# Optimization experiments

Measured on AMD Instinct MI355X. Metric: run time of the kernel, lower is better.

Reference implementation:

```python
import jax, jax.numpy as jnp
import numpy as np

B, NF, QUERY_DIM = 4, 300, 512
HIDDEN, NUM_HEADS = 512, 8
H, W = 80, 80
HEAD_DIM = HIDDEN // NUM_HEADS
NORM_FACT = float(HIDDEN / NUM_HEADS) ** (-0.5)


def setup_inputs() -> dict:
    key = jax.random.key(0)
    k1, k2, k3, k4, k5 = jax.random.split(key, 5)
    # xavier_uniform bound for [HIDDEN, QUERY_DIM] weight
    bound = float(np.sqrt(6.0 / (HIDDEN + QUERY_DIM)))
    return {
        "q": jax.random.normal(k1, (B, NF, QUERY_DIM), dtype=jnp.float32),
        "k": jax.random.normal(k2, (B, QUERY_DIM, H, W), dtype=jnp.float32),
        "mask": jax.random.bernoulli(k3, 0.25, (B, H, W)),  # True = masked out
        "q_w": jax.random.uniform(k4, (HIDDEN, QUERY_DIM), jnp.float32, -bound, bound),
        "q_b": jnp.zeros((HIDDEN,), jnp.float32),
        "k_w": jax.random.uniform(k5, (HIDDEN, QUERY_DIM), jnp.float32, -bound, bound),
        "k_b": jnp.zeros((HIDDEN,), jnp.float32),
    }


def reference(q, k, mask, q_w, q_b, k_w, k_b):
    b, nf, _ = q.shape
    h, w = k.shape[-2], k.shape[-1]
    # q projection: [b, nf, hidden]
    qp = jnp.einsum("bqd,ed->bqe", q, q_w) + q_b
    # k projection (1x1 conv == channel matmul): [b, hidden, h, w]
    kp = jnp.einsum("bdhw,ed->behw", k, k_w) + k_b[None, :, None, None]
    # split heads
    qh = qp.reshape(b, nf, NUM_HEADS, HEAD_DIM) * NORM_FACT   # [b,q,n,c]
    kh = kp.reshape(b, NUM_HEADS, HEAD_DIM, h, w)             # [b,n,c,h,w]
    # batched QK scores (replaces the per-query python loop + cat(dim=2))
    weights = jnp.einsum("bqnc,bnchw->bqnhw", qh, kh)
    weights = weights.reshape(b, 1, nf * NUM_HEADS, h, w)
    # masked_fill with -inf on padded spatial positions
    weights = jnp.where(mask[:, None, None, :, :], -jnp.inf, weights)
    # NOTE: softmax over flatten(2) = jointly over (queries*heads*h*w), as in source
    weights = jax.nn.softmax(weights.reshape(b, 1, -1), axis=-1)
    return weights.reshape(b, 1, nf * NUM_HEADS, h, w)
```

## Files before the change

kernel.cpp:

```cpp
#include <hip/hip_runtime.h>
#include <math.h>

#define B_    4
#define NF    300
#define QD    512
#define HID   512
#define NH    8
#define HD    64
#define HW    6400
#define ROWS  2400
#define PB    15360000
#define NORM_FACT 0.125f
#define NEG_INF (-INFINITY)
#define LDK   40

typedef __bf16 bf16_t;
typedef __bf16 bf16x4_t __attribute__((ext_vector_type(4)));
typedef __bf16 bf16x8_t __attribute__((ext_vector_type(8)));
typedef float  f32x4    __attribute__((ext_vector_type(4)));

__device__ __forceinline__ void splitf(float x, bf16_t& h, bf16_t& l) {
    h = (bf16_t)x;
    l = (bf16_t)(x - (float)h);
}

__global__ __launch_bounds__(256) void qproj_kernel(
    const float* __restrict__ q, const float* __restrict__ qw,
    const float* __restrict__ qb, float* __restrict__ qh)
{
    __shared__ float qs[4][QD];
    const int r0 = blockIdx.x * 4;
    const int t  = threadIdx.x;
    #pragma unroll
    for (int row = 0; row < 4; ++row) {
        qs[row][t]       = q[(size_t)(r0 + row) * QD + t];
        qs[row][t + 256] = q[(size_t)(r0 + row) * QD + t + 256];
    }
    __syncthreads();
    #pragma unroll
    for (int eo = 0; eo < 2; ++eo) {
        const int e = t + eo * 256;
        float a0 = 0.f, a1 = 0.f, a2 = 0.f, a3 = 0.f;
        for (int d = 0; d < QD; d += 4) {
            float4 w = *(const float4*)&qw[(size_t)e * QD + d];
            a0 += qs[0][d]*w.x + qs[0][d+1]*w.y + qs[0][d+2]*w.z + qs[0][d+3]*w.w;
            a1 += qs[1][d]*w.x + qs[1][d+1]*w.y + qs[1][d+2]*w.z + qs[1][d+3]*w.w;
            a2 += qs[2][d]*w.x + qs[2][d+1]*w.y + qs[2][d+2]*w.z + qs[2][d+3]*w.w;
            a3 += qs[3][d]*w.x + qs[3][d+1]*w.y + qs[3][d+2]*w.z + qs[3][d+3]*w.w;
        }
        const float bias = qb[e];
        qh[(size_t)(r0+0)*HID + e] = (a0 + bias) * NORM_FACT;
        qh[(size_t)(r0+1)*HID + e] = (a1 + bias) * NORM_FACT;
        qh[(size_t)(r0+2)*HID + e] = (a2 + bias) * NORM_FACT;
        qh[(size_t)(r0+3)*HID + e] = (a3 + bias) * NORM_FACT;
    }
}

__global__ __launch_bounds__(256) void kproj_mfma(
    const float* __restrict__ k, const float* __restrict__ kw,
    const float* __restrict__ kb, float* __restrict__ kp)
{
    __shared__ __align__(16) bf16_t Ah[128][LDK];
    __shared__ __align__(16) bf16_t Al[128][LDK];
    __shared__ __align__(16) bf16_t Bh[128][LDK];
    __shared__ __align__(16) bf16_t Bl[128][LDK];
    const int b  = blockIdx.z;
    const int e0 = blockIdx.y * 128;
    const int p0 = blockIdx.x * 128;
    const int t  = threadIdx.x;
    const int wave = t >> 6, lane = t & 63;
    const int wr = wave >> 1, wc = wave & 1;
    const int lm = lane & 15, lq = lane >> 4;
    const float* kB = k + (size_t)b * QD * HW;

    f32x4 acc[4][4];
    const f32x4 zero4 = {0.f, 0.f, 0.f, 0.f};
    #pragma unroll
    for (int i = 0; i < 4; ++i)
        #pragma unroll
        for (int j = 0; j < 4; ++j) acc[i][j] = zero4;

    for (int d0 = 0; d0 < QD; d0 += 32) {
        #pragma unroll
        for (int i = 0; i < 4; ++i) {
            int idx = t + i * 256;
            int e = idx >> 3, dp = (idx & 7) << 2;
            float4 v = *(const float4*)&kw[(size_t)(e0 + e) * QD + d0 + dp];
            bf16x4_t hv, lv; bf16_t hx, lx;
            splitf(v.x, hx, lx); hv[0] = hx; lv[0] = lx;
            splitf(v.y, hx, lx); hv[1] = hx; lv[1] = lx;
            splitf(v.z, hx, lx); hv[2] = hx; lv[2] = lx;
            splitf(v.w, hx, lx); hv[3] = hx; lv[3] = lx;
            *(bf16x4_t*)&Ah[e][dp] = hv;
            *(bf16x4_t*)&Al[e][dp] = lv;
        }
        #pragma unroll
        for (int i = 0; i < 4; ++i) {
            int idx = t + i * 256;
            int p = idx & 127, db = (idx >> 7) << 2;
            bf16x4_t hv, lv;
            #pragma unroll
            for (int j = 0; j < 4; ++j) {
                float x = kB[(size_t)(d0 + db + j) * HW + p0 + p];
                bf16_t hx, lx; splitf(x, hx, lx);
                hv[j] = hx; lv[j] = lx;
            }
            *(bf16x4_t*)&Bh[p][db] = hv;
            *(bf16x4_t*)&Bl[p][db] = lv;
        }
        __syncthreads();

        bf16x8_t ah[4], al[4], bh[4], bl[4];
        #pragma unroll
        for (int mt = 0; mt < 4; ++mt) {
            int r = wr * 64 + mt * 16 + lm;
            ah[mt] = *(const bf16x8_t*)&Ah[r][lq * 8];
            al[mt] = *(const bf16x8_t*)&Al[r][lq * 8];
        }
        #pragma unroll
        for (int nt = 0; nt < 4; ++nt) {
            int c = wc * 64 + nt * 16 + lm;
            bh[nt] = *(const bf16x8_t*)&Bh[c][lq * 8];
            bl[nt] = *(const bf16x8_t*)&Bl[c][lq * 8];
        }
        #pragma unroll
        for (int mt = 0; mt < 4; ++mt)
            #pragma unroll
            for (int nt = 0; nt < 4; ++nt) {
                f32x4 a = acc[mt][nt];
                a = __builtin_amdgcn_mfma_f32_16x16x32_bf16(al[mt], bh[nt], a, 0, 0, 0);
                a = __builtin_amdgcn_mfma_f32_16x16x32_bf16(ah[mt], bl[nt], a, 0, 0, 0);
                a = __builtin_amdgcn_mfma_f32_16x16x32_bf16(ah[mt], bh[nt], a, 0, 0, 0);
                acc[mt][nt] = a;
            }
        __syncthreads();
    }

    #pragma unroll
    for (int mt = 0; mt < 4; ++mt) {
        #pragma unroll
        for (int reg = 0; reg < 4; ++reg) {
            int e = e0 + wr * 64 + mt * 16 + lq * 4 + reg;
            float bias = kb[e];
            float* dst = kp + (size_t)b * HID * HW + (size_t)e * HW + p0 + wc * 64 + lm;
            #pragma unroll
            for (int nt = 0; nt < 4; ++nt)
                dst[nt * 16] = acc[mt][nt][reg] + bias;
        }
    }
}

__global__ __launch_bounds__(256) void scores_pass_a(
    const float* __restrict__ qh, const float* __restrict__ kp,
    const int* __restrict__ mask, float* __restrict__ partials)
{
    __shared__ __align__(16) bf16_t Ah[128][LDK];
    __shared__ __align__(16) bf16_t Bh[128][LDK];
    __shared__ float redM[256];
    __shared__ float redS[256];
    const int z  = blockIdx.z;
    const int b  = z >> 3, n = z & 7;
    const int q0 = blockIdx.y * 128;
    const int p0 = blockIdx.x * 128;
    const int t  = threadIdx.x;
    const int wave = t >> 6, lane = t & 63;
    const int wr = wave >> 1, wc = wave & 1;
    const int lm = lane & 15, lq = lane >> 4;

    f32x4 acc[4][4];
    const f32x4 zero4 = {0.f, 0.f, 0.f, 0.f};
    #pragma unroll
    for (int i = 0; i < 4; ++i)
        #pragma unroll
        for (int j = 0; j < 4; ++j) acc[i][j] = zero4;

    for (int d0 = 0; d0 < HD; d0 += 32) {
        #pragma unroll
        for (int i = 0; i < 4; ++i) {
            int idx = t + i * 256;
            int qq = idx >> 3, dp = (idx & 7) << 2;
            int qg = q0 + qq;
            float4 v = make_float4(0.f, 0.f, 0.f, 0.f);
            if (qg < NF)
                v = *(const float4*)&qh[(size_t)(b * NF + qg) * HID + n * HD + d0 + dp];
            bf16x4_t hv;
            hv[0] = (bf16_t)v.x; hv[1] = (bf16_t)v.y;
            hv[2] = (bf16_t)v.z; hv[3] = (bf16_t)v.w;
            *(bf16x4_t*)&Ah[qq][dp] = hv;
        }
        const float* kpB = kp + (size_t)b * HID * HW + (size_t)(n * HD + d0) * HW;
        #pragma unroll
        for (int i = 0; i < 4; ++i) {
            int idx = t + i * 256;
            int p = idx & 127, db = (idx >> 7) << 2;
            bf16x4_t hv;
            #pragma unroll
            for (int j = 0; j < 4; ++j)
                hv[j] = (bf16_t)kpB[(size_t)(db + j) * HW + p0 + p];
            *(bf16x4_t*)&Bh[p][db] = hv;
        }
        __syncthreads();

        bf16x8_t ah[4], bh[4];
        #pragma unroll
        for (int mt = 0; mt < 4; ++mt)
            ah[mt] = *(const bf16x8_t*)&Ah[wr * 64 + mt * 16 + lm][lq * 8];
        #pragma unroll
        for (int nt = 0; nt < 4; ++nt)
            bh[nt] = *(const bf16x8_t*)&Bh[wc * 64 + nt * 16 + lm][lq * 8];
        #pragma unroll
        for (int mt = 0; mt < 4; ++mt)
            #pragma unroll
            for (int nt = 0; nt < 4; ++nt)
                acc[mt][nt] = __builtin_amdgcn_mfma_f32_16x16x32_bf16(
                    ah[mt], bh[nt], acc[mt][nt], 0, 0, 0);
        __syncthreads();
    }

    int mm[4];
    #pragma unroll
    for (int nt = 0; nt < 4; ++nt)
        mm[nt] = mask[b * HW + p0 + wc * 64 + nt * 16 + lm];

    float tm = NEG_INF;
    #pragma unroll
    for (int mt = 0; mt < 4; ++mt) {
        int qbase = q0 + wr * 64 + mt * 16 + lq * 4;
        #pragma unroll
        for (int reg = 0; reg < 4; ++reg) {
            if (qbase + reg < NF) {
                #pragma unroll
                for (int nt = 0; nt < 4; ++nt)
                    if (!mm[nt]) tm = fmaxf(tm, acc[mt][nt][reg]);
            }
        }
    }
    float ts = 0.f;
    if (tm != NEG_INF) {
        #pragma unroll
        for (int mt = 0; mt < 4; ++mt) {
            int qbase = q0 + wr * 64 + mt * 16 + lq * 4;
            #pragma unroll
            for (int reg = 0; reg < 4; ++reg) {
                if (qbase + reg < NF) {
                    #pragma unroll
                    for (int nt = 0; nt < 4; ++nt)
                        if (!mm[nt]) ts += __expf(acc[mt][nt][reg] - tm);
                }
            }
        }
    }

    redM[t] = tm; redS[t] = ts;
    __syncthreads();
    for (int off = 128; off > 0; off >>= 1) {
        if (t < off) {
            float m1 = redM[t],       s1 = redS[t];
            float m2 = redM[t + off], s2 = redS[t + off];
            float M = fmaxf(m1, m2);
            float s = (M == NEG_INF) ? 0.f
                      : (s1 * __expf(m1 - M) + s2 * __expf(m2 - M));
            redM[t] = M; redS[t] = s;
        }
        __syncthreads();
    }
    if (t == 0) {
        int lin = (z * gridDim.y + blockIdx.y) * gridDim.x + blockIdx.x;
        partials[2 * lin]     = redM[0];
        partials[2 * lin + 1] = redS[0];
    }
}

__global__ __launch_bounds__(256) void stats_kernel(
    const float* __restrict__ partials, float* __restrict__ stats, int nper)
{
    __shared__ float redM[256];
    __shared__ float redS[256];
    const int b = blockIdx.x, t = threadIdx.x;
    const float* p = partials + (size_t)b * nper * 2;
    float m = NEG_INF, s = 0.f;
    for (int i = t; i < nper; i += 256) {
        float m2 = p[2 * i], s2 = p[2 * i + 1];
        float M = fmaxf(m, m2);
        float ns = (M == NEG_INF) ? 0.f
                   : (s * __expf(m - M) + s2 * __expf(m2 - M));
        m = M; s = ns;
    }
    redM[t] = m; redS[t] = s;
    __syncthreads();
    for (int off = 128; off > 0; off >>= 1) {
        if (t < off) {
            float m1 = redM[t],       s1 = redS[t];
            float m2 = redM[t + off], s2 = redS[t + off];
            float M = fmaxf(m1, m2);
            float ns = (M == NEG_INF) ? 0.f
                       : (s1 * __expf(m1 - M) + s2 * __expf(m2 - M));
            redM[t] = M; redS[t] = ns;
        }
        __syncthreads();
    }
    if (t == 0) {
        stats[2 * b]     = redM[0];
        stats[2 * b + 1] = 1.0f / redS[0];
    }
}

__global__ __launch_bounds__(256) void scores_pass_b(
    const float* __restrict__ qh, const float* __restrict__ kp,
    const int* __restrict__ mask, const float* __restrict__ stats,
    float* __restrict__ out)
{
    __shared__ __align__(16) bf16_t Ah[128][LDK];
    __shared__ __align__(16) bf16_t Al[128][LDK];
    __shared__ __align__(16) bf16_t Bh[128][LDK];
    __shared__ __align__(16) bf16_t Bl[128][LDK];
    const int z  = blockIdx.z;
    const int b  = z >> 3, n = z & 7;
    const int q0 = blockIdx.y * 128;
    const int p0 = blockIdx.x * 128;
    const int t  = threadIdx.x;
    const int wave = t >> 6, lane = t & 63;
    const int wr = wave >> 1, wc = wave & 1;
    const int lm = lane & 15, lq = lane >> 4;

    const float M    = stats[2 * b];
    const float invS = stats[2 * b + 1];

    f32x4 acc[4][4];
    const f32x4 zero4 = {0.f, 0.f, 0.f, 0.f};
    #pragma unroll
    for (int i = 0; i < 4; ++i)
        #pragma unroll
        for (int j = 0; j < 4; ++j) acc[i][j] = zero4;

    for (int d0 = 0; d0 < HD; d0 += 32) {
        #pragma unroll
        for (int i = 0; i < 4; ++i) {
            int idx = t + i * 256;
            int qq = idx >> 3, dp = (idx & 7) << 2;
            int qg = q0 + qq;
            float4 v = make_float4(0.f, 0.f, 0.f, 0.f);
            if (qg < NF)
                v = *(const float4*)&qh[(size_t)(b * NF + qg) * HID + n * HD + d0 + dp];
            bf16x4_t hv, lv; bf16_t hx, lx;
            splitf(v.x, hx, lx); hv[0] = hx; lv[0] = lx;
            splitf(v.y, hx, lx); hv[1] = hx; lv[1] = lx;
            splitf(v.z, hx, lx); hv[2] = hx; lv[2] = lx;
            splitf(v.w, hx, lx); hv[3] = hx; lv[3] = lx;
            *(bf16x4_t*)&Ah[qq][dp] = hv;
            *(bf16x4_t*)&Al[qq][dp] = lv;
        }
        const float* kpB = kp + (size_t)b * HID * HW + (size_t)(n * HD + d0) * HW;
        #pragma unroll
        for (int i = 0; i < 4; ++i) {
            int idx = t + i * 256;
            int p = idx & 127, db = (idx >> 7) << 2;
            bf16x4_t hv, lv;
            #pragma unroll
            for (int j = 0; j < 4; ++j) {
                float x = kpB[(size_t)(db + j) * HW + p0 + p];
                bf16_t hx, lx; splitf(x, hx, lx);
                hv[j] = hx; lv[j] = lx;
            }
            *(bf16x4_t*)&Bh[p][db] = hv;
            *(bf16x4_t*)&Bl[p][db] = lv;
        }
        __syncthreads();

        bf16x8_t ah[4], al[4], bh[4], bl[4];
        #pragma unroll
        for (int mt = 0; mt < 4; ++mt) {
            int r = wr * 64 + mt * 16 + lm;
            ah[mt] = *(const bf16x8_t*)&Ah[r][lq * 8];
            al[mt] = *(const bf16x8_t*)&Al[r][lq * 8];
        }
        #pragma unroll
        for (int nt = 0; nt < 4; ++nt) {
            int c = wc * 64 + nt * 16 + lm;
            bh[nt] = *(const bf16x8_t*)&Bh[c][lq * 8];
            bl[nt] = *(const bf16x8_t*)&Bl[c][lq * 8];
        }
        #pragma unroll
        for (int mt = 0; mt < 4; ++mt)
            #pragma unroll
            for (int nt = 0; nt < 4; ++nt) {
                f32x4 a = acc[mt][nt];
                a = __builtin_amdgcn_mfma_f32_16x16x32_bf16(al[mt], bh[nt], a, 0, 0, 0);
                a = __builtin_amdgcn_mfma_f32_16x16x32_bf16(ah[mt], bl[nt], a, 0, 0, 0);
                a = __builtin_amdgcn_mfma_f32_16x16x32_bf16(ah[mt], bh[nt], a, 0, 0, 0);
                acc[mt][nt] = a;
            }
        __syncthreads();
    }

    int mm[4];
    #pragma unroll
    for (int nt = 0; nt < 4; ++nt)
        mm[nt] = mask[b * HW + p0 + wc * 64 + nt * 16 + lm];

    #pragma unroll
    for (int mt = 0; mt < 4; ++mt) {
        #pragma unroll
        for (int reg = 0; reg < 4; ++reg) {
            int qg = q0 + wr * 64 + mt * 16 + lq * 4 + reg;
            if (qg < NF) {
                float* dst = out + (size_t)(b * ROWS + qg * NH + n) * HW + p0 + wc * 64 + lm;
                #pragma unroll
                for (int nt = 0; nt < 4; ++nt)
                    dst[nt * 16] = mm[nt] ? 0.f : __expf(acc[mt][nt][reg] - M) * invS;
            }
        }
    }
}

extern "C" void kernel_launch(void* const* d_in, const int* in_sizes, int n_in,
                              void* d_out, int out_size, void* d_ws, size_t ws_size,
                              hipStream_t stream) {
    const float* q    = (const float*)d_in[0];
    const float* k    = (const float*)d_in[1];
    const int*   mask = (const int*)  d_in[2];
    const float* qw   = (const float*)d_in[3];
    const float* qb   = (const float*)d_in[4];
    const float* kw   = (const float*)d_in[5];
    const float* kb   = (const float*)d_in[6];
    float* out = (float*)d_out;
    float* ws  = (float*)d_ws;

    float* qh       = ws;
    float* kp       = ws + 614400;
    float* partials = ws + 13721600;
    float* stats    = ws + 13731200;

    qproj_kernel<<<300, 256, 0, stream>>>(q, qw, qb, qh);
    kproj_mfma<<<dim3(50, 4, 4), 256, 0, stream>>>(k, kw, kb, kp);
    scores_pass_a<<<dim3(50, 3, 32), 256, 0, stream>>>(qh, kp, mask, partials);
    stats_kernel<<<4, 256, 0, stream>>>(partials, stats, 1200);
    scores_pass_b<<<dim3(50, 3, 32), 256, 0, stream>>>(qh, kp, mask, stats, out);
}
```

Baseline: 505.9 us.

## Emit pre-split bf16 head-major swizzled Q/K projections for direct tile loads

The q and k projection kernels now write their outputs as pre-split bf16 hi/lo arrays in a head-major, row-contiguous layout padded to 384 queries, with an XOR swizzle on the 64-wide channel dimension. The two score kernels then copy whole 128x64 tiles into LDS with 16-byte loads and read MFMA fragments through the matching swizzle. This removes the fp32-to-bf16 splitting and the column-strided global gathers that were repeated for every query block, and drops the per-K-step barriers. Pass A now reads only the hi half of the data. In exchange, the projection epilogues do scattered 2-byte stores, and the padded query rows are never written, so they stay uninitialised.

```diff
diff --git a/kernel.cpp b/kernel.cpp
--- a/kernel.cpp
+++ b/kernel.cpp
@@ -9,7 +9,7 @@
 #define HD    64
 #define HW    6400
 #define ROWS  2400
-#define PB    15360000
+#define NQP   384
 #define NORM_FACT 0.125f
 #define NEG_INF (-INFINITY)
 #define LDK   40
@@ -23,14 +23,20 @@
     h = (bf16_t)x;
     l = (bf16_t)(x - (float)h);
 }
+__device__ __forceinline__ int swz(int c, int row) {
+    return (((c >> 3) ^ (row & 7)) << 3) | (c & 7);
+}
 
 __global__ __launch_bounds__(256) void qproj_kernel(
     const float* __restrict__ q, const float* __restrict__ qw,
-    const float* __restrict__ qb, float* __restrict__ qh)
+    const float* __restrict__ qb, bf16_t* __restrict__ qh_hi,
+    bf16_t* __restrict__ qh_lo)
 {
     __shared__ float qs[4][QD];
-    const int r0 = blockIdx.x * 4;
-    const int t  = threadIdx.x;
+    const int r0    = blockIdx.x * 4;
+    const int b     = r0 / NF;
+    const int qbase = r0 % NF;
+    const int t     = threadIdx.x;
     #pragma unroll
     for (int row = 0; row < 4; ++row) {
         qs[row][t]       = q[(size_t)(r0 + row) * QD + t];
@@ -40,25 +46,31 @@
     #pragma unroll
     for (int eo = 0; eo < 2; ++eo) {
         const int e = t + eo * 256;
-        float a0 = 0.f, a1 = 0.f, a2 = 0.f, a3 = 0.f;
+        const int n = e >> 6, c = e & 63;
+        float a[4] = {0.f, 0.f, 0.f, 0.f};
         for (int d = 0; d < QD; d += 4) {
             float4 w = *(const float4*)&qw[(size_t)e * QD + d];
-            a0 += qs[0][d]*w.x + qs[0][d+1]*w.y + qs[0][d+2]*w.z + qs[0][d+3]*w.w;
-            a1 += qs[1][d]*w.x + qs[1][d+1]*w.y + qs[1][d+2]*w.z + qs[1][d+3]*w.w;
-            a2 += qs[2][d]*w.x + qs[2][d+1]*w.y + qs[2][d+2]*w.z + qs[2][d+3]*w.w;
-            a3 += qs[3][d]*w.x + qs[3][d+1]*w.y + qs[3][d+2]*w.z + qs[3][d+3]*w.w;
+            #pragma unroll
+            for (int row = 0; row < 4; ++row)
+                a[row] += qs[row][d]*w.x + qs[row][d+1]*w.y
+                        + qs[row][d+2]*w.z + qs[row][d+3]*w.w;
         }
         const float bias = qb[e];
-        qh[(size_t)(r0+0)*HID + e] = (a0 + bias) * NORM_FACT;
-        qh[(size_t)(r0+1)*HID + e] = (a1 + bias) * NORM_FACT;
-        qh[(size_t)(r0+2)*HID + e] = (a2 + bias) * NORM_FACT;
-        qh[(size_t)(r0+3)*HID + e] = (a3 + bias) * NORM_FACT;
+        #pragma unroll
+        for (int row = 0; row < 4; ++row) {
+            const int qq = qbase + row;
+            const float val = (a[row] + bias) * NORM_FACT;
+            bf16_t h, l; splitf(val, h, l);
+            size_t off = ((size_t)(b * NH + n) * NQP + qq) * 64 + swz(c, qq);
+            qh_hi[off] = h; qh_lo[off] = l;
+        }
     }
 }
 
 __global__ __launch_bounds__(256) void kproj_mfma(
     const float* __restrict__ k, const float* __restrict__ kw,
-    const float* __restrict__ kb, float* __restrict__ kp)
+    const float* __restrict__ kb, bf16_t* __restrict__ kp_hi,
+    bf16_t* __restrict__ kp_lo)
 {
     __shared__ __align__(16) bf16_t Ah[128][LDK];
     __shared__ __align__(16) bf16_t Al[128][LDK];
@@ -84,6 +96,20 @@
         #pragma unroll
         for (int i = 0; i < 4; ++i) {
             int idx = t + i * 256;
+            int p = idx & 127, db = (idx >> 7) << 2;
+            bf16x4_t hv, lv;
+            #pragma unroll
+            for (int j = 0; j < 4; ++j) {
+                float x = kB[(size_t)(d0 + db + j) * HW + p0 + p];
+                bf16_t hx, lx; splitf(x, hx, lx);
+                hv[j] = hx; lv[j] = lx;
+            }
+            *(bf16x4_t*)&Ah[p][db] = hv;
+            *(bf16x4_t*)&Al[p][db] = lv;
+        }
+        #pragma unroll
+        for (int i = 0; i < 4; ++i) {
+            int idx = t + i * 256;
             int e = idx >> 3, dp = (idx & 7) << 2;
             float4 v = *(const float4*)&kw[(size_t)(e0 + e) * QD + d0 + dp];
             bf16x4_t hv, lv; bf16_t hx, lx;
@@ -91,22 +117,8 @@
             splitf(v.y, hx, lx); hv[1] = hx; lv[1] = lx;
             splitf(v.z, hx, lx); hv[2] = hx; lv[2] = lx;
             splitf(v.w, hx, lx); hv[3] = hx; lv[3] = lx;
-            *(bf16x4_t*)&Ah[e][dp] = hv;
-            *(bf16x4_t*)&Al[e][dp] = lv;
-        }
-        #pragma unroll
-        for (int i = 0; i < 4; ++i) {
-            int idx = t + i * 256;
-            int p = idx & 127, db = (idx >> 7) << 2;
-            bf16x4_t hv, lv;
-            #pragma unroll
-            for (int j = 0; j < 4; ++j) {
-                float x = kB[(size_t)(d0 + db + j) * HW + p0 + p];
-                bf16_t hx, lx; splitf(x, hx, lx);
-                hv[j] = hx; lv[j] = lx;
-            }
-            *(bf16x4_t*)&Bh[p][db] = hv;
-            *(bf16x4_t*)&Bl[p][db] = lv;
+            *(bf16x4_t*)&Bh[e][dp] = hv;
+            *(bf16x4_t*)&Bl[e][dp] = lv;
         }
         __syncthreads();
 
@@ -137,25 +149,33 @@
     }
 
     #pragma unroll
-    for (int mt = 0; mt < 4; ++mt) {
-        #pragma unroll
-        for (int reg = 0; reg < 4; ++reg) {
-            int e = e0 + wr * 64 + mt * 16 + lq * 4 + reg;
-            float bias = kb[e];
-            float* dst = kp + (size_t)b * HID * HW + (size_t)e * HW + p0 + wc * 64 + lm;
-            #pragma unroll
-            for (int nt = 0; nt < 4; ++nt)
-                dst[nt * 16] = acc[mt][nt][reg] + bias;
+    for (int nt = 0; nt < 4; ++nt) {
+        const int e = e0 + wc * 64 + nt * 16 + lm;
+        const int n = e >> 6;
+        const int c = (nt * 16 + lm) & 63;
+        const float bias = kb[e];
+        bf16_t* dh = kp_hi + (size_t)(b * NH + n) * HW * 64;
+        bf16_t* dl = kp_lo + (size_t)(b * NH + n) * HW * 64;
+        #pragma unroll
+        for (int mt = 0; mt < 4; ++mt) {
+            #pragma unroll
+            for (int reg = 0; reg < 4; ++reg) {
+                int p = p0 + wr * 64 + mt * 16 + lq * 4 + reg;
+                float val = acc[mt][nt][reg] + bias;
+                bf16_t h, l; splitf(val, h, l);
+                size_t off = (size_t)p * 64 + swz(c, p);
+                dh[off] = h; dl[off] = l;
+            }
         }
     }
 }
 
 __global__ __launch_bounds__(256) void scores_pass_a(
-    const float* __restrict__ qh, const float* __restrict__ kp,
+    const bf16_t* __restrict__ qh_hi, const bf16_t* __restrict__ kp_hi,
     const int* __restrict__ mask, float* __restrict__ partials)
 {
-    __shared__ __align__(16) bf16_t Ah[128][LDK];
-    __shared__ __align__(16) bf16_t Bh[128][LDK];
+    __shared__ __align__(16) bf16_t At[128 * 64];
+    __shared__ __align__(16) bf16_t Bt[128 * 64];
     __shared__ float redM[256];
     __shared__ float redS[256];
     const int z  = blockIdx.z;
@@ -167,6 +187,17 @@
     const int wr = wave >> 1, wc = wave & 1;
     const int lm = lane & 15, lq = lane >> 4;
 
+    const uint4* ga = (const uint4*)(qh_hi + ((size_t)(b * NH + n) * NQP + q0) * 64);
+    const uint4* gb = (const uint4*)(kp_hi + ((size_t)(b * NH + n) * HW  + p0) * 64);
+    uint4* la = (uint4*)At;
+    uint4* lb = (uint4*)Bt;
+    #pragma unroll
+    for (int i = 0; i < 4; ++i) {
+        la[t + i * 256] = ga[t + i * 256];
+        lb[t + i * 256] = gb[t + i * 256];
+    }
+    __syncthreads();
+
     f32x4 acc[4][4];
     const f32x4 zero4 = {0.f, 0.f, 0.f, 0.f};
     #pragma unroll
@@ -174,47 +205,25 @@
         #pragma unroll
         for (int j = 0; j < 4; ++j) acc[i][j] = zero4;
 
-    for (int d0 = 0; d0 < HD; d0 += 32) {
-        #pragma unroll
-        for (int i = 0; i < 4; ++i) {
-            int idx = t + i * 256;
-            int qq = idx >> 3, dp = (idx & 7) << 2;
-            int qg = q0 + qq;
-            float4 v = make_float4(0.f, 0.f, 0.f, 0.f);
-            if (qg < NF)
-                v = *(const float4*)&qh[(size_t)(b * NF + qg) * HID + n * HD + d0 + dp];
-            bf16x4_t hv;
-            hv[0] = (bf16_t)v.x; hv[1] = (bf16_t)v.y;
-            hv[2] = (bf16_t)v.z; hv[3] = (bf16_t)v.w;
-            *(bf16x4_t*)&Ah[qq][dp] = hv;
-        }
-        const float* kpB = kp + (size_t)b * HID * HW + (size_t)(n * HD + d0) * HW;
-        #pragma unroll
-        for (int i = 0; i < 4; ++i) {
-            int idx = t + i * 256;
-            int p = idx & 127, db = (idx >> 7) << 2;
-            bf16x4_t hv;
-            #pragma unroll
-            for (int j = 0; j < 4; ++j)
-                hv[j] = (bf16_t)kpB[(size_t)(db + j) * HW + p0 + p];
-            *(bf16x4_t*)&Bh[p][db] = hv;
-        }
-        __syncthreads();
-
-        bf16x8_t ah[4], bh[4];
-        #pragma unroll
-        for (int mt = 0; mt < 4; ++mt)
-            ah[mt] = *(const bf16x8_t*)&Ah[wr * 64 + mt * 16 + lm][lq * 8];
-        #pragma unroll
-        for (int nt = 0; nt < 4; ++nt)
-            bh[nt] = *(const bf16x8_t*)&Bh[wc * 64 + nt * 16 + lm][lq * 8];
+    #pragma unroll
+    for (int ks = 0; ks < 2; ++ks) {
+        bf16x8_t af[4], bf[4];
+        #pragma unroll
+        for (int mt = 0; mt < 4; ++mt) {
+            int row = wr * 64 + mt * 16 + lm;
+            af[mt] = *(const bf16x8_t*)&At[row * 64 + (((lq + ks * 4) ^ (lm & 7)) << 3)];
+        }
+        #pragma unroll
+        for (int nt = 0; nt < 4; ++nt) {
+            int row = wc * 64 + nt * 16 + lm;
+            bf[nt] = *(const bf16x8_t*)&Bt[row * 64 + (((lq + ks * 4) ^ (lm & 7)) << 3)];
+        }
         #pragma unroll
         for (int mt = 0; mt < 4; ++mt)
             #pragma unroll
             for (int nt = 0; nt < 4; ++nt)
                 acc[mt][nt] = __builtin_amdgcn_mfma_f32_16x16x32_bf16(
-                    ah[mt], bh[nt], acc[mt][nt], 0, 0, 0);
-        __syncthreads();
+                    af[mt], bf[nt], acc[mt][nt], 0, 0, 0);
     }
 
     int mm[4];
@@ -306,14 +315,15 @@
 }
 
 __global__ __launch_bounds__(256) void scores_pass_b(
-    const float* __restrict__ qh, const float* __restrict__ kp,
+    const bf16_t* __restrict__ qh_hi, const bf16_t* __restrict__ qh_lo,
+    const bf16_t* __restrict__ kp_hi, const bf16_t* __restrict__ kp_lo,
     const int* __restrict__ mask, const float* __restrict__ stats,
     float* __restrict__ out)
 {
-    __shared__ __align__(16) bf16_t Ah[128][LDK];
-    __shared__ __align__(16) bf16_t Al[128][LDK];
-    __shared__ __align__(16) bf16_t Bh[128][LDK];
-    __shared__ __align__(16) bf16_t Bl[128][LDK];
+    __shared__ __align__(16) bf16_t Aht[128 * 64];
+    __shared__ __align__(16) bf16_t Alt[128 * 64];
+    __shared__ __align__(16) bf16_t Bht[128 * 64];
+    __shared__ __align__(16) bf16_t Blt[128 * 64];
     const int z  = blockIdx.z;
     const int b  = z >> 3, n = z & 7;
     const int q0 = blockIdx.y * 128;
@@ -326,6 +336,21 @@
     const float M    = stats[2 * b];
     const float invS = stats[2 * b + 1];
 
+    const size_t abase = ((size_t)(b * NH + n) * NQP + q0) * 64;
+    const size_t bbase = ((size_t)(b * NH + n) * HW  + p0) * 64;
+    const uint4* gah = (const uint4*)(qh_hi + abase);
+    const uint4* gal = (const uint4*)(qh_lo + abase);
+    const uint4* gbh = (const uint4*)(kp_hi + bbase);
+    const uint4* gbl = (const uint4*)(kp_lo + bbase);
+    #pragma unroll
+    for (int i = 0; i < 4; ++i) {
+        ((uint4*)Aht)[t + i * 256] = gah[t + i * 256];
+        ((uint4*)Alt)[t + i * 256] = gal[t + i * 256];
+        ((uint4*)Bht)[t + i * 256] = gbh[t + i * 256];
+        ((uint4*)Blt)[t + i * 256] = gbl[t + i * 256];
+    }
+    __syncthreads();
+
     f32x4 acc[4][4];
     const f32x4 zero4 = {0.f, 0.f, 0.f, 0.f};
     #pragma unroll
@@ -333,52 +358,22 @@
         #pragma unroll
         for (int j = 0; j < 4; ++j) acc[i][j] = zero4;
 
-    for (int d0 = 0; d0 < HD; d0 += 32) {
-        #pragma unroll
-        for (int i = 0; i < 4; ++i) {
-            int idx = t + i * 256;
-            int qq = idx >> 3, dp = (idx & 7) << 2;
-            int qg = q0 + qq;
-            float4 v = make_float4(0.f, 0.f, 0.f, 0.f);
-            if (qg < NF)
-                v = *(const float4*)&qh[(size_t)(b * NF + qg) * HID + n * HD + d0 + dp];
-            bf16x4_t hv, lv; bf16_t hx, lx;
-            splitf(v.x, hx, lx); hv[0] = hx; lv[0] = lx;
-            splitf(v.y, hx, lx); hv[1] = hx; lv[1] = lx;
-            splitf(v.z, hx, lx); hv[2] = hx; lv[2] = lx;
-            splitf(v.w, hx, lx); hv[3] = hx; lv[3] = lx;
-            *(bf16x4_t*)&Ah[qq][dp] = hv;
-            *(bf16x4_t*)&Al[qq][dp] = lv;
-        }
-        const float* kpB = kp + (size_t)b * HID * HW + (size_t)(n * HD + d0) * HW;
-        #pragma unroll
-        for (int i = 0; i < 4; ++i) {
-            int idx = t + i * 256;
-            int p = idx & 127, db = (idx >> 7) << 2;
-            bf16x4_t hv, lv;
-            #pragma unroll
-            for (int j = 0; j < 4; ++j) {
-                float x = kpB[(size_t)(db + j) * HW + p0 + p];
-                bf16_t hx, lx; splitf(x, hx, lx);
-                hv[j] = hx; lv[j] = lx;
-            }
-            *(bf16x4_t*)&Bh[p][db] = hv;
-            *(bf16x4_t*)&Bl[p][db] = lv;
-        }
-        __syncthreads();
-
+    #pragma unroll
+    for (int ks = 0; ks < 2; ++ks) {
         bf16x8_t ah[4], al[4], bh[4], bl[4];
         #pragma unroll
         for (int mt = 0; mt < 4; ++mt) {
-            int r = wr * 64 + mt * 16 + lm;
-            ah[mt] = *(const bf16x8_t*)&Ah[r][lq * 8];
-            al[mt] = *(const bf16x8_t*)&Al[r][lq * 8];
+            int row = wr * 64 + mt * 16 + lm;
+            int off = row * 64 + (((lq + ks * 4) ^ (lm & 7)) << 3);
+            ah[mt] = *(const bf16x8_t*)&Aht[off];
+            al[mt] = *(const bf16x8_t*)&Alt[off];
         }
         #pragma unroll
         for (int nt = 0; nt < 4; ++nt) {
-            int c = wc * 64 + nt * 16 + lm;
-            bh[nt] = *(const bf16x8_t*)&Bh[c][lq * 8];
-            bl[nt] = *(const bf16x8_t*)&Bl[c][lq * 8];
+            int row = wc * 64 + nt * 16 + lm;
+            int off = row * 64 + (((lq + ks * 4) ^ (lm & 7)) << 3);
+            bh[nt] = *(const bf16x8_t*)&Bht[off];
+            bl[nt] = *(const bf16x8_t*)&Blt[off];
         }
         #pragma unroll
         for (int mt = 0; mt < 4; ++mt)
@@ -390,7 +385,6 @@
                 a = __builtin_amdgcn_mfma_f32_16x16x32_bf16(ah[mt], bh[nt], a, 0, 0, 0);
                 acc[mt][nt] = a;
             }
-        __syncthreads();
     }
 
     int mm[4];
@@ -424,16 +418,18 @@
     const float* kw   = (const float*)d_in[5];
     const float* kb   = (const float*)d_in[6];
     float* out = (float*)d_out;
-    float* ws  = (float*)d_ws;
-
-    float* qh       = ws;
-    float* kp       = ws + 614400;
-    float* partials = ws + 13721600;
-    float* stats    = ws + 13731200;
-
-    qproj_kernel<<<300, 256, 0, stream>>>(q, qw, qb, qh);
-    kproj_mfma<<<dim3(50, 4, 4), 256, 0, stream>>>(k, kw, kb, kp);
-    scores_pass_a<<<dim3(50, 3, 32), 256, 0, stream>>>(qh, kp, mask, partials);
+
+    bf16_t* kp_hi = (bf16_t*)d_ws;
+    bf16_t* kp_lo = kp_hi + (size_t)B_ * NH * HW * 64;
+    bf16_t* qh_hi = kp_lo + (size_t)B_ * NH * HW * 64;
+    bf16_t* qh_lo = qh_hi + (size_t)B_ * NH * NQP * 64;
+    float* partials = (float*)(qh_lo + (size_t)B_ * NH * NQP * 64);
+    float* stats    = partials + 2 * 4800;
+
+    qproj_kernel<<<300, 256, 0, stream>>>(q, qw, qb, qh_hi, qh_lo);
+    kproj_mfma<<<dim3(50, 4, 4), 256, 0, stream>>>(k, kw, kb, kp_hi, kp_lo);
+    scores_pass_a<<<dim3(50, 3, 32), 256, 0, stream>>>(qh_hi, kp_hi, mask, partials);
     stats_kernel<<<4, 256, 0, stream>>>(partials, stats, 1200);
-    scores_pass_b<<<dim3(50, 3, 32), 256, 0, stream>>>(qh, kp, mask, stats, out);
-}
+    scores_pass_b<<<dim3(50, 3, 32), 256, 0, stream>>>(qh_hi, qh_lo, kp_hi, kp_lo,
+                                                       mask, stats, out);
+}
```

New measurement: 503.6 us. About the same (-0.5%).
